# Performance work log

Measured on AMD Instinct MI355X. Metric: run time of the kernel, lower is better.

The kernel has to match this reference:

```python
import jax, jax.numpy as jnp
import numpy as np

CHUNK = 64
MIN_CLAMP = 1e-6
EPS = 1e-5


def layer_norm(x, scale, bias):
    mu = jnp.mean(x, axis=-1, keepdims=True)
    var = jnp.var(x, axis=-1, keepdims=True)
    return (x - mu) / jnp.sqrt(var + EPS) * scale + bias


def group_norm(x, scale, bias, num_groups):
    # Faithful to the module's GroupNorm: stats over (all rows, within-group channels)
    shp = x.shape
    xr = x.reshape(-1, num_groups, shp[-1] // num_groups)
    mu = jnp.mean(xr, axis=(0, 2), keepdims=True)
    var = jnp.var(xr, axis=(0, 2), keepdims=True)
    xn = ((xr - mu) / jnp.sqrt(var + EPS)).reshape(shp)
    return xn * scale + bias


def time_shift(x):
    return jnp.pad(x[:, :-1], ((0, 0), (1, 0), (0, 0)))


def chunkwise_single(k, v, r, w, u, state):
    # one (batch*head) lane: k,v,r,w,u are (L, D); state is (D, D)
    C = CHUNK
    L, D = r.shape
    pad = (-L) % C
    if pad:
        padf = lambda a: jnp.pad(a, ((0, pad), (0, 0)))
        r, k, v, w, u = map(padf, (r, k, v, w, u))
    Lp = L + pad
    N = Lp // C
    r, k, v, w, u = (a.reshape(N, C, D) for a in (r, k, v, w, u))
    w = jnp.log(jnp.clip(w, MIN_CLAMP, 1.0))
    A = jnp.exp(jnp.cumsum(w, axis=1))                                    # (N,C,D)
    A_inter = jnp.exp(jax.lax.cumsum(w, axis=1, reverse=True) - w)        # (N,C,D)
    A_intra = jnp.cumsum(w, axis=1)                                       # (N,C,D)
    kv = jnp.einsum('ncj,nck->ncjk', A_inter * k, v)                      # (N,C,D,D)

    def scan_fn(s, inp):
        A_t, kv_t = inp
        return A_t * s + kv_t, s

    new_state, S = jax.lax.scan(scan_fn, state, (A.reshape(Lp, D), kv.reshape(Lp, D, D)))
    S = S.reshape(N, C, D, D)
    inter = jnp.einsum('ncj,ncjk->nck', r * jnp.exp(A_intra - w), S)

    mid = C // 2

    def intra_fn(rc, kc, vc, Ac, uc):
        r_decay = rc * jnp.exp(jnp.pad(Ac[:-1], ((1, 0), (0, 0))) - Ac[mid:mid + 1])
        k_decay = kc * jnp.exp(Ac[mid:mid + 1] - Ac)
        u_diag = jnp.diag(jnp.sum(rc * uc * kc, -1))
        return (jnp.tril(r_decay @ k_decay.T, -1) + u_diag) @ vc

    intra = jax.vmap(intra_fn)(r, k, v, A_intra, u)
    y = (inter + intra).reshape(Lp, D)[:L]
    return y, new_state


def _forward(x, state, time_maa_x, time_maa_w, time_maa_k, time_maa_v, time_maa_r, time_maa_g,
             time_decay, time_faaaa, time_maa_w1, time_maa_w2, time_decay_w1, time_decay_w2,
             Wr, Wk, Wv, Wg, Wo, ln_x_scale, ln_x_bias,
             time_maa_k_ch, time_maa_r_ch, Wk_ch, Wv_ch, Wr_ch,
             ln1_scale, ln1_bias, ln2_scale, ln2_bias):
    B, T, E = x.shape
    H, Sh = time_faaaa.shape
    # ---- time mixing (on ln1(x)) ----
    xn = layer_norm(x, ln1_scale, ln1_bias)
    sx = time_shift(xn) - xn
    xmix = xn + sx * time_maa_x
    t5 = jnp.tanh(xmix @ time_maa_w1).reshape(B, T, 5, -1).swapaxes(1, 2)    # (B,5,T,32)
    # faithful to original: batched matmul then reshape (B,5,T,E) -> (5,B,T,E)
    m = jnp.einsum('bgtc,gce->bgte', t5, time_maa_w2).reshape(5, B, T, E)
    mw, mk, mv, mr, mg = m
    xw = xn + sx * (time_maa_w + mw)
    xk = xn + sx * (time_maa_k + mk)
    xv = xn + sx * (time_maa_v + mv)
    xr = xn + sx * (time_maa_r + mr)
    xg = xn + sx * (time_maa_g + mg)
    r = (xr @ Wr).reshape(B, T, H, Sh)
    k = (xk @ Wk).reshape(B, T, H, Sh)
    v = (xv @ Wv).reshape(B, T, H, Sh)
    g = jax.nn.silu(xg @ Wg)                                                 # (B,T,H*Sh)
    off = (jnp.tanh(xw @ time_decay_w1) @ time_decay_w2).reshape(B, T, H, Sh)
    w = jax.nn.softplus(-(time_decay.reshape(1, 1, H, Sh) + off))
    u = jnp.broadcast_to(time_faaaa, (B, T, H, Sh))
    lane = lambda a: a.transpose(0, 2, 1, 3).reshape(B * H, T, Sh)
    y, new_state = jax.vmap(chunkwise_single)(lane(k), lane(v), lane(r), lane(w), lane(u),
                                              state.reshape(B * H, Sh, Sh))
    y = y.reshape(B, H, T, Sh).transpose(0, 2, 1, 3).reshape(B, T, H * Sh)
    y = group_norm(y, ln_x_scale, ln_x_bias, H)
    x = x + (y * g) @ Wo
    # ---- channel mixing (on ln2(x)) ----
    xn2 = layer_norm(x, ln2_scale, ln2_bias)
    sx2 = time_shift(xn2) - xn2
    kk = jax.nn.relu((xn2 + sx2 * time_maa_k_ch) @ Wk_ch) ** 2
    kv = kk @ Wv_ch
    out = x + jax.nn.sigmoid((xn2 + sx2 * time_maa_r_ch) @ Wr_ch) * kv
    return out, new_state.reshape(B, H, Sh, Sh)


def setup_inputs():
    B, T, E = 2, 512, 1024
    H, Sh, F = 16, 64, 4096
    D = H * Sh
    layer_id, n_layer = 12, 24
    r01 = layer_id / (n_layer - 1)
    r10 = 1.0 - layer_id / n_layer
    ar_e = np.arange(E, dtype=np.float64) / E
    maa = lambda p: jnp.asarray((1.0 - ar_e ** p).reshape(1, 1, E), jnp.float32)
    n = np.arange(D, dtype=np.float64)
    time_decay = jnp.asarray((-6 + 5 * (n / (D - 1)) ** (0.7 + 1.3 * r01)).reshape(1, D), jnp.float32)
    time_faaaa = jnp.asarray((r01 * (1 - n / (D - 1)) + ((n + 1) % 3 - 1) * 0.1).reshape(H, Sh), jnp.float32)
    key = jax.random.key(0)
    ks = jax.random.split(key, 14)
    uni = lambda kk, shp: jax.random.uniform(kk, shp, jnp.float32, 0.0, 1e-4)
    dense = lambda kk, i, o: jax.random.normal(kk, (i, o), jnp.float32) / np.float32(np.sqrt(i))
    return dict(
        x=jax.random.normal(ks[0], (B, T, E), jnp.float32),
        state=jnp.zeros((B, H, Sh, Sh), jnp.float32),
        time_maa_x=maa(r10), time_maa_w=maa(r10), time_maa_k=maa(r10),
        time_maa_v=maa(r10 + 0.3 * r01), time_maa_r=maa(0.5 * r10), time_maa_g=maa(0.5 * r10),
        time_decay=time_decay, time_faaaa=time_faaaa,
        time_maa_w1=uni(ks[1], (E, 5 * 32)), time_maa_w2=uni(ks[2], (5, 32, E)),
        time_decay_w1=uni(ks[3], (E, 64)), time_decay_w2=uni(ks[4], (64, E)),
        Wr=dense(ks[5], E, D), Wk=dense(ks[6], E, D), Wv=dense(ks[7], E, D),
        Wg=dense(ks[8], E, D), Wo=dense(ks[9], D, E),
        ln_x_scale=jnp.ones((D,), jnp.float32), ln_x_bias=jnp.zeros((D,), jnp.float32),
        time_maa_k_ch=maa(r10), time_maa_r_ch=maa(r10),
        Wk_ch=dense(ks[10], E, F), Wv_ch=dense(ks[11], F, E), Wr_ch=dense(ks[12], E, E),
        ln1_scale=jnp.ones((E,), jnp.float32), ln1_bias=jnp.zeros((E,), jnp.float32),
        ln2_scale=jnp.ones((E,), jnp.float32), ln2_bias=jnp.zeros((E,), jnp.float32),
    )


def reference(x, state, time_maa_x, time_maa_w, time_maa_k, time_maa_v, time_maa_r, time_maa_g,
              time_decay, time_faaaa, time_maa_w1, time_maa_w2, time_decay_w1, time_decay_w2,
              Wr, Wk, Wv, Wg, Wo, ln_x_scale, ln_x_bias,
              time_maa_k_ch, time_maa_r_ch, Wk_ch, Wv_ch, Wr_ch,
              ln1_scale, ln1_bias, ln2_scale, ln2_bias):
    return _forward(x, state, time_maa_x, time_maa_w, time_maa_k, time_maa_v, time_maa_r, time_maa_g,
                    time_decay, time_faaaa, time_maa_w1, time_maa_w2, time_decay_w1, time_decay_w2,
                    Wr, Wk, Wv, Wg, Wo, ln_x_scale, ln_x_bias,
                    time_maa_k_ch, time_maa_r_ch, Wk_ch, Wv_ch, Wr_ch,
                    ln1_scale, ln1_bias, ln2_scale, ln2_bias)
```

## Files before the change

kernel.cpp:

```cpp
#include <hip/hip_runtime.h>
#include <math.h>

#define T_  512
#define E_  1024
#define BTE 1048576

enum { EPI_NONE=0, EPI_TANH=1, EPI_SILU=2, EPI_RELU2=3, EPI_WLOG=4, EPI_ADDRES=5,
       EPI_SIGMUL4=6 };

typedef __attribute__((ext_vector_type(8))) short bf16x8;
typedef __attribute__((ext_vector_type(4))) float f32x4;

__device__ __forceinline__ unsigned short f2bf(float f) {
    union { float f; unsigned u; } v; v.f = f;
    unsigned r = v.u + 0x7fffu + ((v.u >> 16) & 1u);
    return (unsigned short)(r >> 16);
}
__device__ __forceinline__ float bf2f(unsigned short h) {
    union { unsigned u; float f; } v; v.u = ((unsigned)h) << 16;
    return v.f;
}

__global__ __launch_bounds__(256) void ln1mix_k(const float* __restrict__ x,
        const float* __restrict__ sc, const float* __restrict__ bi,
        const float* __restrict__ maa,
        float* __restrict__ xn, unsigned short* __restrict__ xmix)
{
    const int row = blockIdx.x;
    const int t = row & 511;
    const int tid = threadIdx.x;
    const float* xr = x + (size_t)row * E_;
    float4 v = *reinterpret_cast<const float4*>(xr + tid*4);
    float4 vp = make_float4(0.f, 0.f, 0.f, 0.f);
    if (t) vp = *reinterpret_cast<const float4*>(xr - E_ + tid*4);
    float s   = v.x + v.y + v.z + v.w;
    float ss  = v.x*v.x + v.y*v.y + v.z*v.z + v.w*v.w;
    float sp  = vp.x + vp.y + vp.z + vp.w;
    float ssp = vp.x*vp.x + vp.y*vp.y + vp.z*vp.z + vp.w*vp.w;
    #pragma unroll
    for (int off = 32; off > 0; off >>= 1) {
        s   += __shfl_down(s, off);
        ss  += __shfl_down(ss, off);
        sp  += __shfl_down(sp, off);
        ssp += __shfl_down(ssp, off);
    }
    __shared__ float p0[4], p1[4], p2[4], p3[4];
    __shared__ float st[4];
    if ((tid & 63) == 0) { p0[tid>>6]=s; p1[tid>>6]=ss; p2[tid>>6]=sp; p3[tid>>6]=ssp; }
    __syncthreads();
    if (tid == 0) {
        float S  = p0[0]+p0[1]+p0[2]+p0[3];
        float SS = p1[0]+p1[1]+p1[2]+p1[3];
        float Sp = p2[0]+p2[1]+p2[2]+p2[3];
        float SSp= p3[0]+p3[1]+p3[2]+p3[3];
        float mu  = S * (1.f/E_);
        float var = SS * (1.f/E_) - mu*mu;
        float mup = Sp * (1.f/E_);
        float varp= SSp * (1.f/E_) - mup*mup;
        st[0] = mu; st[1] = rsqrtf(var + 1e-5f);
        st[2] = mup; st[3] = rsqrtf(varp + 1e-5f);
    }
    __syncthreads();
    const float mu = st[0], rstd = st[1], mup = st[2], rstdp = st[3];
    float4 s4 = *reinterpret_cast<const float4*>(sc + tid*4);
    float4 b4 = *reinterpret_cast<const float4*>(bi + tid*4);
    float xnv[4], prv[4];
    xnv[0]=(v.x-mu)*rstd*s4.x+b4.x; xnv[1]=(v.y-mu)*rstd*s4.y+b4.y;
    xnv[2]=(v.z-mu)*rstd*s4.z+b4.z; xnv[3]=(v.w-mu)*rstd*s4.w+b4.w;
    prv[0]=t?(vp.x-mup)*rstdp*s4.x+b4.x:0.f; prv[1]=t?(vp.y-mup)*rstdp*s4.y+b4.y:0.f;
    prv[2]=t?(vp.z-mup)*rstdp*s4.z+b4.z:0.f; prv[3]=t?(vp.w-mup)*rstdp*s4.w+b4.w:0.f;
    float4 o; o.x=xnv[0]; o.y=xnv[1]; o.z=xnv[2]; o.w=xnv[3];
    *reinterpret_cast<float4*>(xn + (size_t)row*E_ + tid*4) = o;
    #pragma unroll
    for (int j = 0; j < 4; ++j) {
        int e = tid*4 + j;
        xmix[(size_t)row*E_ + e] = f2bf(xnv[j] + (prv[j]-xnv[j])*maa[e]);
    }
}

__global__ __launch_bounds__(256) void ln2mix_k(const float* __restrict__ x2,
        const float* __restrict__ sc, const float* __restrict__ bi,
        const float* __restrict__ maaK, const float* __restrict__ maaR,
        unsigned short* __restrict__ ak, unsigned short* __restrict__ ar)
{
    const int row = blockIdx.x;
    const int t = row & 511;
    const int tid = threadIdx.x;
    const float* xr = x2 + (size_t)row * E_;
    float4 v = *reinterpret_cast<const float4*>(xr + tid*4);
    float4 vp = make_float4(0.f, 0.f, 0.f, 0.f);
    if (t) vp = *reinterpret_cast<const float4*>(xr - E_ + tid*4);
    float s   = v.x + v.y + v.z + v.w;
    float ss  = v.x*v.x + v.y*v.y + v.z*v.z + v.w*v.w;
    float sp  = vp.x + vp.y + vp.z + vp.w;
    float ssp = vp.x*vp.x + vp.y*vp.y + vp.z*vp.z + vp.w*vp.w;
    #pragma unroll
    for (int off = 32; off > 0; off >>= 1) {
        s   += __shfl_down(s, off);
        ss  += __shfl_down(ss, off);
        sp  += __shfl_down(sp, off);
        ssp += __shfl_down(ssp, off);
    }
    __shared__ float p0[4], p1[4], p2[4], p3[4];
    __shared__ float st[4];
    if ((tid & 63) == 0) { p0[tid>>6]=s; p1[tid>>6]=ss; p2[tid>>6]=sp; p3[tid>>6]=ssp; }
    __syncthreads();
    if (tid == 0) {
        float S  = p0[0]+p0[1]+p0[2]+p0[3];
        float SS = p1[0]+p1[1]+p1[2]+p1[3];
        float Sp = p2[0]+p2[1]+p2[2]+p2[3];
        float SSp= p3[0]+p3[1]+p3[2]+p3[3];
        float mu  = S * (1.f/E_);
        float var = SS * (1.f/E_) - mu*mu;
        float mup = Sp * (1.f/E_);
        float varp= SSp * (1.f/E_) - mup*mup;
        st[0] = mu; st[1] = rsqrtf(var + 1e-5f);
        st[2] = mup; st[3] = rsqrtf(varp + 1e-5f);
    }
    __syncthreads();
    const float mu = st[0], rstd = st[1], mup = st[2], rstdp = st[3];
    float4 s4 = *reinterpret_cast<const float4*>(sc + tid*4);
    float4 b4 = *reinterpret_cast<const float4*>(bi + tid*4);
    float xnv[4], prv[4];
    xnv[0]=(v.x-mu)*rstd*s4.x+b4.x; xnv[1]=(v.y-mu)*rstd*s4.y+b4.y;
    xnv[2]=(v.z-mu)*rstd*s4.z+b4.z; xnv[3]=(v.w-mu)*rstd*s4.w+b4.w;
    prv[0]=t?(vp.x-mup)*rstdp*s4.x+b4.x:0.f; prv[1]=t?(vp.y-mup)*rstdp*s4.y+b4.y:0.f;
    prv[2]=t?(vp.z-mup)*rstdp*s4.z+b4.z:0.f; prv[3]=t?(vp.w-mup)*rstdp*s4.w+b4.w:0.f;
    #pragma unroll
    for (int j = 0; j < 4; ++j) {
        int e = tid*4 + j;
        float sxv = prv[j] - xnv[j];
        ak[(size_t)row*E_ + e] = f2bf(xnv[j] + sxv*maaK[e]);
        ar[(size_t)row*E_ + e] = f2bf(xnv[j] + sxv*maaR[e]);
    }
}

__global__ __launch_bounds__(256) void t5red_k(const float* __restrict__ tp,
        unsigned short* __restrict__ t5p)
{
    int idx = blockIdx.x*256 + threadIdx.x;
    int c = idx & 63, bt = (idx >> 6) & 1023, g = idx >> 16;
    unsigned short o = 0;
    if (c < 32) {
        float s = 0.f;
        size_t off = (size_t)bt*160 + g*32 + c;
        #pragma unroll
        for (int z = 0; z < 8; ++z) s += tp[(size_t)z*163840 + off];
        o = f2bf(tanhf(s));
    }
    t5p[idx] = o;
}

__global__ __launch_bounds__(256) void dw1red_k(const float* __restrict__ dp,
        unsigned short* __restrict__ h)
{
    int idx = blockIdx.x*256 + threadIdx.x;
    float s = 0.f;
    #pragma unroll
    for (int z = 0; z < 8; ++z) s += dp[(size_t)z*65536 + idx];
    h[idx] = f2bf(tanhf(s));
}

__global__ __launch_bounds__(256) void mix5_apply_k(const float* __restrict__ xn,
        const unsigned short* __restrict__ mb,
        const float* __restrict__ maaW, const float* __restrict__ maaK,
        const float* __restrict__ maaV, const float* __restrict__ maaR,
        const float* __restrict__ maaG,
        unsigned short* __restrict__ xw, unsigned short* __restrict__ xk,
        unsigned short* __restrict__ xv, unsigned short* __restrict__ xr,
        unsigned short* __restrict__ xg)
{
    int idx = blockIdx.x*256 + threadIdx.x;
    int e = idx & 1023;
    int bt = idx >> 10;
    int b = bt >> 9, t = bt & 511;
    float xnv = xn[idx];
    float prev = t ? xn[idx - E_] : 0.f;
    float sxv = prev - xnv;
    float m[5];
    #pragma unroll
    for (int o = 0; o < 5; ++o) {
        int L = o*2 + b;
        int bs = L / 5, gs = L - bs*5;
        m[o] = bf2f(mb[(size_t)gs*1048576 + (size_t)(bs*T_ + t)*E_ + e]);
    }
    xw[idx] = f2bf(xnv + sxv*(maaW[e] + m[0]));
    xk[idx] = f2bf(xnv + sxv*(maaK[e] + m[1]));
    xv[idx] = f2bf(xnv + sxv*(maaV[e] + m[2]));
    xr[idx] = f2bf(xnv + sxv*(maaR[e] + m[3]));
    xg[idx] = f2bf(xnv + sxv*(maaG[e] + m[4]));
}

struct WTA {
    const float* src[16];
    unsigned short* dst[16];
    int K[16], N[16], Npad[16], Kpad[16], tx[16];
    int cum[17];
};
__global__ __launch_bounds__(256) void wtransall_k(WTA a)
{
    int bid = blockIdx.x;
    int s = 0;
    while (bid >= a.cum[s+1]) ++s;
    const int local = bid - a.cum[s];
    const int bx = local % a.tx[s];
    const int by = local / a.tx[s];
    const float* S = a.src[s];
    unsigned short* D = a.dst[s];
    const int K = a.K[s], N = a.N[s], Npad = a.Npad[s], Kpad = a.Kpad[s];
    __shared__ float t[64][65];
    const int tid = threadIdx.x;
    const int k0 = by*64, n0 = bx*64;
    #pragma unroll
    for (int i = 0; i < 16; ++i) {
        int r = i*4 + (tid >> 6), c = tid & 63;
        int gk = k0 + r, gn = n0 + c;
        t[r][c] = (gk < K && gn < N) ? S[(size_t)gk*N + gn] : 0.f;
    }
    __syncthreads();
    #pragma unroll
    for (int i = 0; i < 16; ++i) {
        int r = i*4 + (tid >> 6), c = tid & 63;
        int gn = n0 + r, gk = k0 + c;
        if (gn < Npad && gk < Kpad)
            D[(size_t)gn*Kpad + gk] = f2bf(t[c][r]);
    }
}

struct GemmArgs {
    const unsigned short* A[8];
    const unsigned short* B[8];
    void* C[8];
    const float* p1[8];
    const float* p2[8];
    int epi[8];
    int obf[8];
    int k0[8];
    int M, N, K, ldK;
};
__global__ __launch_bounds__(256) void mgemm_k(GemmArgs g)
{
    const int bz = blockIdx.z;
    const unsigned short* Ag = g.A[bz];
    const unsigned short* BT = g.B[bz];
    const int N = g.N, K = g.K;
    const int gx = gridDim.x, gy = gridDim.y;
    const int lin = blockIdx.x + gx*blockIdx.y;
    const int q = (gx*gy) >> 3;
    const int tile = (lin & 7)*q + (lin >> 3);
    const int bx = tile / gy;
    const int by = tile - bx*gy;
    const int m0 = by * 64, n0 = bx * 64;
    const int tid = threadIdx.x;
    const int lane = tid & 63, w = tid >> 6;

    __shared__ __align__(16) unsigned short As[2][4096];
    __shared__ __align__(16) unsigned short Bs[2][4096];

    const size_t rowBytes = (size_t)g.ldK * 2;
    int sI[4], sIsB[4]; size_t sOff[4];
    #pragma unroll
    for (int ii = 0; ii < 4; ++ii) {
        int t = w*4 + ii;
        int isB = t >> 3;
        int i = t & 7;
        int r = i*8 + (lane >> 3);
        int gb = ((lane & 7) * 16) ^ ((r & 7) << 4);
        sI[ii] = i; sIsB[ii] = isB;
        int srow = (isB ? n0 : m0) + r;
        sOff[ii] = (size_t)srow * rowBytes + gb;
    }
    auto stage = [&](int buf, size_t kbyte) {
        #pragma unroll
        for (int ii = 0; ii < 4; ++ii) {
            const char* src = (const char*)(sIsB[ii] ? BT : Ag) + sOff[ii] + kbyte;
            unsigned short* dst = (sIsB[ii] ? Bs[buf] : As[buf]) + sI[ii]*512;
            auto g1 = (const __attribute__((address_space(1))) unsigned int*)(src);
            auto l3 = (__attribute__((address_space(3))) unsigned int*)(uintptr_t)(dst);
            __builtin_amdgcn_global_load_lds(g1, l3, 16, 0, 0);
        }
    };

    const int wm = (w >> 1) * 32, wn = (w & 1) * 32;
    const int lr = lane & 15, lk = lane >> 4;
    int aoff[2][2], boff[2][2];
    #pragma unroll
    for (int mi = 0; mi < 2; ++mi)
        #pragma unroll
        for (int kw = 0; kw < 2; ++kw) {
            int ar = wm + mi*16 + lr;
            aoff[mi][kw] = ar*128 + ((kw*64 + lk*16) ^ ((ar & 7) << 4));
            int br = wn + mi*16 + lr;
            boff[mi][kw] = br*128 + ((kw*64 + lk*16) ^ ((br & 7) << 4));
        }

    f32x4 acc[2][2] = {};
    const size_t kbase = (size_t)g.k0[bz] * 2;
    stage(0, kbase);
    const int nk = K >> 6;
    int cur = 0;
    for (int kt = 0; kt < nk; ++kt) {
        __syncthreads();
        if (kt + 1 < nk) stage(cur ^ 1, kbase + (size_t)(kt + 1) * 128);
        const char* Ab = (const char*)As[cur];
        const char* Bb = (const char*)Bs[cur];
        bf16x8 af[2][2], bfv[2][2];
        #pragma unroll
        for (int mi = 0; mi < 2; ++mi)
            #pragma unroll
            for (int kw = 0; kw < 2; ++kw) {
                af[mi][kw]  = *(const bf16x8*)(Ab + aoff[mi][kw]);
                bfv[mi][kw] = *(const bf16x8*)(Bb + boff[mi][kw]);
            }
        #pragma unroll
        for (int kw = 0; kw < 2; ++kw)
            #pragma unroll
            for (int mi = 0; mi < 2; ++mi)
                #pragma unroll
                for (int ni = 0; ni < 2; ++ni)
                    acc[mi][ni] = __builtin_amdgcn_mfma_f32_16x16x32_bf16(
                        af[mi][kw], bfv[ni][kw], acc[mi][ni], 0, 0, 0);
        cur ^= 1;
    }

    const int epi = g.epi[bz], obf = g.obf[bz];
    const float* p1 = g.p1[bz];
    const float* p2 = g.p2[bz];
    float* Cf = (float*)g.C[bz];
    unsigned short* Ch = (unsigned short*)g.C[bz];
    #pragma unroll
    for (int mi = 0; mi < 2; ++mi) {
        #pragma unroll
        for (int ni = 0; ni < 2; ++ni) {
            #pragma unroll
            for (int j = 0; j < 4; ++j) {
                int gm = m0 + wm + mi*16 + lk*4 + j;
                int gn = n0 + wn + ni*16 + lr;
                if (gn >= N) continue;
                size_t idx = (size_t)gm * N + gn;
                float a = acc[mi][ni][j];
                float o = a;
                if (epi == EPI_TANH)        o = tanhf(a);
                else if (epi == EPI_SILU)   o = a / (1.f + expf(-a));
                else if (epi == EPI_RELU2)  { float r = fmaxf(a, 0.f); o = r*r; }
                else if (epi == EPI_WLOG) {
                    float z = -(p1[gn] + a);
                    float sp = (z > 15.f) ? z : log1pf(expf(z));
                    o = logf(fminf(fmaxf(sp, 1e-6f), 1.f));
                }
                else if (epi == EPI_ADDRES) o = a + p1[idx];
                else if (epi == EPI_SIGMUL4) {
                    float kvs = p1[idx] + p1[idx + BTE] + p1[idx + 2*BTE] + p1[idx + 3*BTE];
                    o = p2[idx] + kvs / (1.f + expf(-a));
                }
                if (obf) Ch[idx] = f2bf(o); else Cf[idx] = o;
            }
        }
    }
}

#define SWZI(r, c)  (((r) << 6) + ((c) ^ (((r) & 7) << 3)))
#define FIDX(r, kw) (((r) << 6) + ((((kw)*32) + fk*8) ^ (((r) & 7) << 3)))
__global__ __launch_bounds__(1024, 4) void chunk1_k(
    const unsigned short* __restrict__ rb, const unsigned short* __restrict__ kb,
    const unsigned short* __restrict__ vb,
    const unsigned short* __restrict__ hdecb, const unsigned short* __restrict__ dw2T,
    const float* __restrict__ tdecay, const float* __restrict__ faaaa,
    float* __restrict__ ypart, unsigned short* __restrict__ Ug,
    unsigned short* __restrict__ RDimg, unsigned short* __restrict__ BFb,
    float* __restrict__ B63g)
{
    const int blk = blockIdx.x;
    const int bh = blk >> 3, nc = blk & 7;
    const int b = bh >> 4, h = bh & 15;
    const int tid = threadIdx.x;
    const int l = tid & 63, w = tid >> 6;
    const int jl = l, q = w;
    const int fr = l & 15, fk = l >> 4;
    const int wm = (w >> 2) * 16, wn = (w & 3) * 16;
    const int t0 = nc * 64;

    __shared__ float sQS[16][64];
    __shared__ float sUD[64];
    __shared__ __align__(16) unsigned short pool[32768];
    unsigned short* sRDb  = pool;
    unsigned short* sKAb  = pool + 4096;
    unsigned short* sKA2b = pool + 8192;
    unsigned short* sKATb = pool + 12288;
    unsigned short* sVTb  = pool + 16384;
    unsigned short* sVXTb = pool + 20480;
    unsigned short* sQMb  = pool + 24576;
    unsigned short* sPMb  = pool + 28672;
    float* wlogf = (float*)(pool + 12288);

    const float u_reg = faaaa[h*64 + jl];
    const size_t base = (size_t)b*T_*E_ + (size_t)h*64;
    const size_t coff = (size_t)blk * 4096;

    {
        const int isB = w >> 3;
        const int i = w & 7;
        const int r = i*8 + (l >> 3);
        const int gb = ((l & 7)*16) ^ ((r & 7) << 4);
        const char* src = isB
            ? ((const char*)dw2T  + (size_t)(h*64 + r)*128 + gb)
            : ((const char*)hdecb + (size_t)(b*T_ + t0 + r)*128 + gb);
        unsigned short* dst = (isB ? sPMb : sQMb) + i*512;
        auto g1 = (const __attribute__((address_space(1))) unsigned int*)(src);
        auto l3 = (__attribute__((address_space(3))) unsigned int*)(uintptr_t)(dst);
        __builtin_amdgcn_global_load_lds(g1, l3, 16, 0, 0);
    }
    __syncthreads();

    {
        f32x4 accO = {};
        #pragma unroll
        for (int kw = 0; kw < 2; ++kw) {
            bf16x8 aH = *(const bf16x8*)(&sQMb[FIDX(wm + fr, kw)]);
            bf16x8 bD = *(const bf16x8*)(&sPMb[FIDX(wn + fr, kw)]);
            accO = __builtin_amdgcn_mfma_f32_16x16x32_bf16(aH, bD, accO, 0,0,0);
        }
        const float td = tdecay[h*64 + wn + fr];
        #pragma unroll
        for (int reg = 0; reg < 4; ++reg) {
            const int t = wm + fk*4 + reg;
            const int col = wn + fr;
            float z = -(td + accO[reg]);
            float sp = (z > 15.f) ? z : log1pf(expf(z));
            wlogf[t*64 + col] = logf(fminf(fmaxf(sp, 1e-6f), 1.f));
        }
    }
    __syncthreads();

    float loc[4], vreg[4];
    {
        float cum = 0.f;
        #pragma unroll
        for (int c = 0; c < 4; ++c) {
            float wv = wlogf[(q*4 + c)*64 + jl];
            cum += wv; loc[c] = cum;
        }
        sQS[q][jl] = cum;
    }
    __syncthreads();
    float pre = 0.f, atot = 0.f;
    #pragma unroll
    for (int qq = 0; qq < 16; ++qq) {
        float v = sQS[qq][jl];
        atot += v;
        if (qq < q) pre += v;
    }

    #pragma unroll
    for (int c = 0; c < 4; ++c) {
        const int t = q*4 + c;
        const size_t gi = base + (size_t)(t0 + t)*E_ + jl;
        const float rv = bf2f(rb[gi]), kv = bf2f(kb[gi]), vv = bf2f(vb[gi]);
        vreg[c] = vv;
        const float a = loc[c] + pre;
        const float aprev = (c > 0) ? (loc[c-1] + pre) : pre;
        sRDb [SWZI(t, jl)] = f2bf(rv * expf(aprev));
        const float ka = kv * expf(atot - a);
        sKAb [SWZI(t, jl)] = f2bf(ka);
        sKA2b[SWZI(t, jl)] = f2bf(kv * expf(-a));
        sKATb[SWZI(jl, t)] = f2bf(ka);
        sVTb [SWZI(jl, t)] = f2bf(vv);
        float p = rv * u_reg * kv;
        #pragma unroll
        for (int off = 32; off > 0; off >>= 1) p += __shfl_down(p, off);
        if (jl == 0) sUD[t] = p;
    }
    __syncthreads();

    f32x4 accQ = {}, accP = {};
    #pragma unroll
    for (int kw = 0; kw < 2; ++kw) {
        bf16x8 ar  = *(const bf16x8*)(&sRDb [FIDX(wm + fr, kw)]);
        bf16x8 bka = *(const bf16x8*)(&sKAb [FIDX(wn + fr, kw)]);
        bf16x8 bk2 = *(const bf16x8*)(&sKA2b[FIDX(wn + fr, kw)]);
        accQ = __builtin_amdgcn_mfma_f32_16x16x32_bf16(ar, bk2, accQ, 0,0,0);
        accP = __builtin_amdgcn_mfma_f32_16x16x32_bf16(ar, bka, accP, 0,0,0);
    }
    #pragma unroll
    for (int reg = 0; reg < 4; ++reg) {
        int t = wm + fk*4 + reg;
        int s = wn + fr;
        float qv = (s < t) ? accQ[reg] : ((s == t) ? sUD[t] : 0.f);
        float pv = (s < t) ? accP[reg] : 0.f;
        sQMb[SWZI(t, s)] = f2bf(qv);
        sPMb[SWZI(t, s)] = f2bf(pv);
    }

    float loc2[4];
    {
        float cum2 = 0.f;
        #pragma unroll
        for (int c = 0; c < 4; ++c) {
            cum2 += loc[c] + pre;
            loc2[c] = cum2;
        }
        sQS[q][jl] = cum2;
    }
    __syncthreads();
    {
        float pre2 = 0.f;
        #pragma unroll
        for (int qq = 0; qq < 16; ++qq) if (qq < q) pre2 += sQS[qq][jl];
        #pragma unroll
        for (int c = 0; c < 4; ++c) {
            const int t = q*4 + c;
            const float Bv = loc2[c] + pre2;
            const float Bprev = (c > 0) ? (loc2[c-1] + pre2) : pre2;
            const unsigned short bfh = f2bf(expf(Bprev));
            sKA2b[t*64 + jl] = bfh;
            BFb[coff + t*64 + jl] = bfh;
            sVXTb[SWZI(jl, t)] = f2bf(vreg[c] * expf(-Bv));
            if (t == 63) B63g[(size_t)blk*64 + jl] = expf(Bv);
        }
    }
    __syncthreads();

    {
        f32x4 accI = {}, accL = {}, accU = {};
        #pragma unroll
        for (int kw = 0; kw < 2; ++kw) {
            bf16x8 aQ = *(const bf16x8*)(&sQMb [FIDX(wm + fr, kw)]);
            bf16x8 aP = *(const bf16x8*)(&sPMb [FIDX(wm + fr, kw)]);
            bf16x8 aK = *(const bf16x8*)(&sKATb[FIDX(wm + fr, kw)]);
            bf16x8 bV = *(const bf16x8*)(&sVTb [FIDX(wn + fr, kw)]);
            bf16x8 bX = *(const bf16x8*)(&sVXTb[FIDX(wn + fr, kw)]);
            accI = __builtin_amdgcn_mfma_f32_16x16x32_bf16(aQ, bV, accI, 0,0,0);
            accL = __builtin_amdgcn_mfma_f32_16x16x32_bf16(aP, bX, accL, 0,0,0);
            accU = __builtin_amdgcn_mfma_f32_16x16x32_bf16(aK, bX, accU, 0,0,0);
        }
        #pragma unroll
        for (int reg = 0; reg < 4; ++reg) {
            int t = wm + fk*4 + reg;
            int k = wn + fr;
            float bfv = bf2f(sKA2b[t*64 + k]);
            ypart[base + (size_t)(t0 + t)*E_ + k] = accI[reg] + bfv*accL[reg];
            Ug[coff + t*64 + k] = f2bf(accU[reg]);
        }
    }
    if (tid < 512)
        ((bf16x8*)(RDimg + coff))[tid] = ((const bf16x8*)sRDb)[tid];
}

__global__ __launch_bounds__(256) void chunk2_k(
    const float* __restrict__ st_in, const unsigned short* __restrict__ Ug,
    const float* __restrict__ B63g,
    unsigned short* __restrict__ Simg, float* __restrict__ st_out)
{
    const int bh = blockIdx.x;
    const int tid = threadIdx.x;
    __shared__ float S[4096];
    for (int i = tid; i < 4096; i += 256) S[i] = st_in[(size_t)bh*4096 + i];
    __syncthreads();
    const int k = tid >> 2, j0 = (tid & 3) * 16;
    for (int nc = 0; nc < 8; ++nc) {
        const size_t coff = ((size_t)bh*8 + nc) * 4096;
        #pragma unroll
        for (int hf = 0; hf < 2; ++hf) {
            bf16x8 tmp;
            #pragma unroll
            for (int e = 0; e < 8; ++e) tmp[e] = (short)f2bf(S[(j0 + hf*8 + e)*64 + k]);
            *(bf16x8*)(&Simg[coff + SWZI(k, j0 + hf*8)]) = tmp;
        }
        __syncthreads();
        for (int i = tid; i < 4096; i += 256) {
            int kk = i & 63;
            S[i] = B63g[((size_t)bh*8 + nc)*64 + kk] * (S[i] + bf2f(Ug[coff + i]));
        }
        __syncthreads();
    }
    for (int i = tid; i < 4096; i += 256) st_out[(size_t)bh*4096 + i] = S[i];
}

__global__ __launch_bounds__(256) void chunk3_k(
    const unsigned short* __restrict__ RDimg, const unsigned short* __restrict__ Simg,
    const unsigned short* __restrict__ BFb, float* __restrict__ yb,
    float* __restrict__ part)
{
    const int blk = blockIdx.x;
    const int bh = blk >> 3, nc = blk & 7;
    const int b = bh >> 4, h = bh & 15;
    const int tid = threadIdx.x;
    const int l = tid & 63, w = tid >> 6;
    const int fr = l & 15, fk = l >> 4;
    const int wm = (w >> 1) * 32, wn = (w & 1) * 32;
    const int t0 = nc * 64;
    __shared__ __align__(16) unsigned short sRDb[4096];
    __shared__ __align__(16) unsigned short sSTb[4096];
    const size_t coff = (size_t)blk * 4096;

    #pragma unroll
    for (int ii = 0; ii < 2; ++ii) {
        int seg = (w*2 + ii) * 512;
        {
            auto g1 = (const __attribute__((address_space(1))) unsigned int*)(RDimg + coff + seg + (l << 3));
            auto l3 = (__attribute__((address_space(3))) unsigned int*)(uintptr_t)(sRDb + seg);
            __builtin_amdgcn_global_load_lds(g1, l3, 16, 0, 0);
        }
        {
            auto g1 = (const __attribute__((address_space(1))) unsigned int*)(Simg + coff + seg + (l << 3));
            auto l3 = (__attribute__((address_space(3))) unsigned int*)(uintptr_t)(sSTb + seg);
            __builtin_amdgcn_global_load_lds(g1, l3, 0x10, 0, 0);
        }
    }
    __syncthreads();

    f32x4 accS[2][2] = {};
    #pragma unroll
    for (int kw = 0; kw < 2; ++kw) {
        bf16x8 aR[2], bS[2];
        #pragma unroll
        for (int mi = 0; mi < 2; ++mi)
            aR[mi] = *(const bf16x8*)(&sRDb[FIDX(wm + mi*16 + fr, kw)]);
        #pragma unroll
        for (int ni = 0; ni < 2; ++ni)
            bS[ni] = *(const bf16x8*)(&sSTb[FIDX(wn + ni*16 + fr, kw)]);
        #pragma unroll
        for (int mi = 0; mi < 2; ++mi)
            #pragma unroll
            for (int ni = 0; ni < 2; ++ni)
                accS[mi][ni] = __builtin_amdgcn_mfma_f32_16x16x32_bf16(aR[mi], bS[ni], accS[mi][ni], 0,0,0);
    }
    const size_t base = (size_t)b*T_*E_ + (size_t)h*64;
    float s = 0.f, ss = 0.f;
    #pragma unroll
    for (int mi = 0; mi < 2; ++mi)
        #pragma unroll
        for (int ni = 0; ni < 2; ++ni)
            #pragma unroll
            for (int reg = 0; reg < 4; ++reg) {
                int t = wm + mi*16 + fk*4 + reg;
                int k = wn + ni*16 + fr;
                size_t gp = base + (size_t)(t0 + t)*E_ + k;
                float yv = yb[gp] + bf2f(BFb[coff + t*64 + k]) * accS[mi][ni][reg];
                yb[gp] = yv;
                s += yv; ss += yv*yv;
            }
    #pragma unroll
    for (int off = 32; off > 0; off >>= 1) {
        s  += __shfl_down(s, off);
        ss += __shfl_down(ss, off);
    }
    __shared__ float ps[4], pss[4];
    if (l == 0) { ps[w] = s; pss[w] = ss; }
    __syncthreads();
    if (tid == 0) {
        part[blk]       = ps[0]+ps[1]+ps[2]+ps[3];
        part[256 + blk] = pss[0]+pss[1]+pss[2]+pss[3];
    }
}

__global__ __launch_bounds__(256) void gn_apply_k(const float* __restrict__ y,
        const float* __restrict__ g, const float* __restrict__ part,
        const float* __restrict__ sc, const float* __restrict__ bi,
        unsigned short* __restrict__ z)
{
    __shared__ float smu[16], srs[16];
    const int tid = threadIdx.x;
    if (tid < 16) {
        float s = 0.f, ss = 0.f;
        #pragma unroll
        for (int b = 0; b < 2; ++b)
            #pragma unroll
            for (int ncc = 0; ncc < 8; ++ncc) {
                int ib = (b*16 + tid)*8 + ncc;
                s  += part[ib];
                ss += part[256 + ib];
            }
        float mu  = s * (1.f/65536.f);
        float var = ss * (1.f/65536.f) - mu*mu;
        smu[tid] = mu;
        srs[tid] = rsqrtf(var + 1e-5f);
    }
    __syncthreads();
    int idx = blockIdx.x*256 + tid;
    int d = idx & 1023;
    int h = d >> 6;
    float yn = (y[idx] - smu[h])*srs[h]*sc[d] + bi[d];
    z[idx] = f2bf(yn * g[idx]);
}

extern "C" void kernel_launch(void* const* d_in, const int* in_sizes, int n_in,
                              void* d_out, int out_size, void* d_ws, size_t ws_size,
                              hipStream_t stream)
{
    const float* x       = (const float*)d_in[0];
    const float* state0  = (const float*)d_in[1];
    const float* maa_x   = (const float*)d_in[2];
    const float* maa_w   = (const float*)d_in[3];
    const float* maa_k   = (const float*)d_in[4];
    const float* maa_v   = (const float*)d_in[5];
    const float* maa_r   = (const float*)d_in[6];
    const float* maa_g   = (const float*)d_in[7];
    const float* tdecay  = (const float*)d_in[8];
    const float* faaaa   = (const float*)d_in[9];
    const float* w1      = (const float*)d_in[10];
    const float* w2      = (const float*)d_in[11];
    const float* dw1     = (const float*)d_in[12];
    const float* dw2     = (const float*)d_in[13];
    const float* Wr      = (const float*)d_in[14];
    const float* Wk      = (const float*)d_in[15];
    const float* Wv      = (const float*)d_in[16];
    const float* Wg      = (const float*)d_in[17];
    const float* Wo      = (const float*)d_in[18];
    const float* lnx_s   = (const float*)d_in[19];
    const float* lnx_b   = (const float*)d_in[20];
    const float* maa_kch = (const float*)d_in[21];
    const float* maa_rch = (const float*)d_in[22];
    const float* Wk_ch   = (const float*)d_in[23];
    const float* Wv_ch   = (const float*)d_in[24];
    const float* Wr_ch   = (const float*)d_in[25];
    const float* ln1_s   = (const float*)d_in[26];
    const float* ln1_b   = (const float*)d_in[27];
    const float* ln2_s   = (const float*)d_in[28];
    const float* ln2_b   = (const float*)d_in[29];

    float* xn     = (float*)d_ws;
    float* t5dead = xn + 1048576;
    float* gbuf   = t5dead + 163840;
    float* wlogb  = gbuf + 1048576;
    float* ybuf   = wlogb + 1048576;
    float* kvb    = ybuf + 1048576;
    float* gnpart = kvb + 1048576;
    float* gnstat = gnpart + 1024;
    float* b63g   = gnstat + 32;
    unsigned short* u = (unsigned short*)(b63g + 16384);
    unsigned short* xmix = u;  u += 1048576;
    unsigned short* xw   = u;  u += 1048576;
    unsigned short* xk   = u;  u += 1048576;
    unsigned short* xv_  = u;  u += 1048576;
    unsigned short* xr   = u;  u += 1048576;
    unsigned short* xg   = u;  u += 1048576;
    unsigned short* xtr  = u;  u += 1048576;
    unsigned short* rb   = u;  u += 1048576;
    unsigned short* kb   = u;  u += 1048576;
    unsigned short* vb   = u;  u += 1048576;
    unsigned short* hdecb= u;  u += 65536;
    unsigned short* WrT  = u;  u += 1048576;
    unsigned short* WkT  = u;  u += 1048576;
    unsigned short* WvT  = u;  u += 1048576;
    unsigned short* WgT  = u;  u += 1048576;
    unsigned short* WoT  = u;  u += 1048576;
    unsigned short* WrchT= u;  u += 1048576;
    unsigned short* WkchT= u;  u += 4194304;
    unsigned short* WvchT= u;  u += 4194304;
    unsigned short* w1T  = u;  u += 196608;
    unsigned short* dw1T = u;  u += 65536;
    unsigned short* dw2T = u;  u += 65536;
    unsigned short* W2T5 = u;  u += 327680;
    unsigned short* t5p  = u;  u += 327680;
    unsigned short* zbuf  = xmix;
    unsigned short* akb   = xw;
    unsigned short* arb   = xk;
    unsigned short* kkb   = xv_;
    unsigned short* mb16  = (unsigned short*)wlogb;
    unsigned short* Ug    = xv_;
    unsigned short* RDimg = xg;
    unsigned short* Simg  = xtr;
    unsigned short* BFb   = xmix;
    float* tpart = gbuf;
    float* dpart = (float*)xmix;
    float* kpart = gbuf;

    float* out   = (float*)d_out;
    float* x2buf = out;
    float* stout = out + (size_t)BTE;

    {
        WTA a{};
        const float* srcs[16] = {Wr, Wk, Wv, Wg, Wo, Wr_ch, Wk_ch, Wv_ch, w1, dw1, dw2,
                                 w2, w2+32768, w2+65536, w2+98304, w2+131072};
        unsigned short* dsts[16] = {WrT, WkT, WvT, WgT, WoT, WrchT, WkchT, WvchT,
                                    w1T, dw1T, dw2T,
                                    W2T5, W2T5+65536, W2T5+131072, W2T5+196608, W2T5+262144};
        int Ks[16]    = {1024,1024,1024,1024,1024,1024, 1024, 4096, 1024, 1024,   64, 32,32,32,32,32};
        int Ns[16]    = {1024,1024,1024,1024,1024,1024, 4096, 1024,  160,   64, 1024, 1024,1024,1024,1024,1024};
        int Npads[16] = {1024,1024,1024,1024,1024,1024, 4096, 1024,  192,   64, 1024, 1024,1024,1024,1024,1024};
        int Kpads[16] = {1024,1024,1024,1024,1024,1024, 1024, 4096, 1024, 1024,   64, 64,64,64,64,64};
        int cum = 0;
        for (int i = 0; i < 16; ++i) {
            a.src[i] = srcs[i]; a.dst[i] = dsts[i];
            a.K[i] = Ks[i]; a.N[i] = Ns[i]; a.Npad[i] = Npads[i]; a.Kpad[i] = Kpads[i];
            int txc = (Ns[i] + 63) / 64;
            int tyc = (Ks[i] + 63) / 64;
            a.tx[i] = txc;
            a.cum[i] = cum;
            cum += txc * tyc;
        }
        a.cum[16] = cum;
        wtransall_k<<<cum, 256, 0, stream>>>(a);
    }

    ln1mix_k<<<1024, 256, 0, stream>>>(x, ln1_s, ln1_b, maa_x, xn, xmix);
    { GemmArgs g{}; g.M=1024; g.N=160; g.K=128; g.ldK=1024;
      for (int z = 0; z < 8; ++z) {
          g.A[z]=xmix; g.B[z]=w1T; g.C[z]=tpart + (size_t)z*163840;
          g.epi[z]=EPI_NONE; g.obf[z]=0; g.k0[z]=z*128;
      }
      mgemm_k<<<dim3(3,16,8), 256, 0, stream>>>(g); }
    t5red_k<<<1280, 256, 0, stream>>>(tpart, t5p);
    { GemmArgs g{}; g.M=1024; g.N=1024; g.K=64; g.ldK=64;
      for (int z = 0; z < 5; ++z) {
          g.A[z]=t5p + (size_t)z*65536; g.B[z]=W2T5 + (size_t)z*65536;
          g.C[z]=mb16 + (size_t)z*1048576; g.epi[z]=EPI_NONE; g.obf[z]=1;
      }
      mgemm_k<<<dim3(16,16,5), 256, 0, stream>>>(g); }
    mix5_apply_k<<<4096, 256, 0, stream>>>(xn, mb16, maa_w, maa_k, maa_v, maa_r, maa_g,
                                           xw, xk, xv_, xr, xg);
    { GemmArgs g{}; g.M=1024; g.N=1024; g.K=1024; g.ldK=1024;
      g.A[0]=xr;  g.B[0]=WrT; g.C[0]=rb;   g.epi[0]=EPI_NONE; g.obf[0]=1;
      g.A[1]=xk;  g.B[1]=WkT; g.C[1]=kb;   g.epi[1]=EPI_NONE; g.obf[1]=1;
      g.A[2]=xv_; g.B[2]=WvT; g.C[2]=vb;   g.epi[2]=EPI_NONE; g.obf[2]=1;
      g.A[3]=xg;  g.B[3]=WgT; g.C[3]=gbuf; g.epi[3]=EPI_SILU; g.obf[3]=0;
      mgemm_k<<<dim3(16,16,4), 256, 0, stream>>>(g); }
    { GemmArgs g{}; g.M=1024; g.N=64; g.K=128; g.ldK=1024;
      for (int z = 0; z < 8; ++z) {
          g.A[z]=xw; g.B[z]=dw1T; g.C[z]=dpart + (size_t)z*65536;
          g.epi[z]=EPI_NONE; g.obf[z]=0; g.k0[z]=z*128;
      }
      mgemm_k<<<dim3(1,16,8), 256, 0, stream>>>(g); }
    dw1red_k<<<256, 256, 0, stream>>>(dpart, hdecb);

    chunk1_k<<<256, 1024, 0, stream>>>(rb, kb, vb, hdecb, dw2T, tdecay, faaaa,
                                       ybuf, Ug, RDimg, BFb, b63g);
    chunk2_k<<<32, 256, 0, stream>>>(state0, Ug, b63g, Simg, stout);
    chunk3_k<<<256, 256, 0, stream>>>(RDimg, Simg, BFb, ybuf, gnpart);

    gn_apply_k<<<4096, 256, 0, stream>>>(ybuf, gbuf, gnpart, lnx_s, lnx_b, zbuf);
    { GemmArgs g{}; g.M=1024; g.N=1024; g.K=1024; g.ldK=1024;
      g.A[0]=zbuf; g.B[0]=WoT; g.C[0]=x2buf; g.epi[0]=EPI_ADDRES; g.obf[0]=0; g.p1[0]=x;
      mgemm_k<<<dim3(16,16,1), 256, 0, stream>>>(g); }

    ln2mix_k<<<1024, 256, 0, stream>>>(x2buf, ln2_s, ln2_b, maa_kch, maa_rch, akb, arb);
    { GemmArgs g{}; g.M=1024; g.N=4096; g.K=1024; g.ldK=1024;
      g.A[0]=akb; g.B[0]=WkchT; g.C[0]=kkb; g.epi[0]=EPI_RELU2; g.obf[0]=1;
      mgemm_k<<<dim3(64,16,1), 256, 0, stream>>>(g); }
    { GemmArgs g{}; g.M=1024; g.N=1024; g.K=1024; g.ldK=4096;
      for (int z = 0; z < 4; ++z) {
          g.A[z]=kkb; g.B[z]=WvchT; g.C[z]=kpart + (size_t)z*BTE;
          g.epi[z]=EPI_NONE; g.obf[z]=0; g.k0[z]=z*1024;
      }
      mgemm_k<<<dim3(16,16,4), 256, 0, stream>>>(g); }
    { GemmArgs g{}; g.M=1024; g.N=1024; g.K=1024; g.ldK=1024;
      g.A[0]=arb; g.B[0]=WrchT; g.C[0]=out; g.epi[0]=EPI_SIGMUL4; g.obf[0]=0;
      g.p1[0]=kpart; g.p2[0]=x2buf;
      mgemm_k<<<dim3(16,16,1), 256, 0, stream>>>(g); }
}
```

Baseline: 186.1 us.

## Split-K the output projection GEMM and fold reduction plus residual into ln2mix

Result: no change. 184.9 us (median of 2 runs) (-0.7%).

```diff
diff --git a/kernel.cpp b/kernel.cpp
--- a/kernel.cpp
+++ b/kernel.cpp
@@ -78,38 +78,52 @@
     }
 }
 
-__global__ __launch_bounds__(256) void ln2mix_k(const float* __restrict__ x2,
+__global__ __launch_bounds__(256) void ln2mix_k(const float* __restrict__ pa,
+        const float* __restrict__ pb, const float* __restrict__ xres,
         const float* __restrict__ sc, const float* __restrict__ bi,
         const float* __restrict__ maaK, const float* __restrict__ maaR,
+        float* __restrict__ x2out,
         unsigned short* __restrict__ ak, unsigned short* __restrict__ ar)
 {
     const int row = blockIdx.x;
     const int t = row & 511;
     const int tid = threadIdx.x;
-    const float* xr = x2 + (size_t)row * E_;
-    float4 v = *reinterpret_cast<const float4*>(xr + tid*4);
+    const size_t off = (size_t)row*E_ + tid*4;
+    float4 a0 = *reinterpret_cast<const float4*>(pa + off);
+    float4 a1 = *reinterpret_cast<const float4*>(pb + off);
+    float4 xv = *reinterpret_cast<const float4*>(xres + off);
+    float4 v;
+    v.x = a0.x + a1.x + xv.x; v.y = a0.y + a1.y + xv.y;
+    v.z = a0.z + a1.z + xv.z; v.w = a0.w + a1.w + xv.w;
     float4 vp = make_float4(0.f, 0.f, 0.f, 0.f);
-    if (t) vp = *reinterpret_cast<const float4*>(xr - E_ + tid*4);
+    if (t) {
+        float4 b0 = *reinterpret_cast<const float4*>(pa + off - E_);
+        float4 b1 = *reinterpret_cast<const float4*>(pb + off - E_);
+        float4 bx = *reinterpret_cast<const float4*>(xres + off - E_);
+        vp.x = b0.x + b1.x + bx.x; vp.y = b0.y + b1.y + bx.y;
+        vp.z = b0.z + b1.z + bx.z; vp.w = b0.w + b1.w + bx.w;
+    }
+    *reinterpret_cast<float4*>(x2out + off) = v;
     float s   = v.x + v.y + v.z + v.w;
     float ss  = v.x*v.x + v.y*v.y + v.z*v.z + v.w*v.w;
     float sp  = vp.x + vp.y + vp.z + vp.w;
     float ssp = vp.x*vp.x + vp.y*vp.y + vp.z*vp.z + vp.w*vp.w;
     #pragma unroll
-    for (int off = 32; off > 0; off >>= 1) {
-        s   += __shfl_down(s, off);
-        ss  += __shfl_down(ss, off);
-        sp  += __shfl_down(sp, off);
-        ssp += __shfl_down(ssp, off);
-    }
-    __shared__ float p0[4], p1[4], p2[4], p3[4];
+    for (int off2 = 32; off2 > 0; off2 >>= 1) {
+        s   += __shfl_down(s, off2);
+        ss  += __shfl_down(ss, off2);
+        sp  += __shfl_down(sp, off2);
+        ssp += __shfl_down(ssp, off2);
+    }
+    __shared__ float q0[4], q1[4], q2[4], q3[4];
     __shared__ float st[4];
-    if ((tid & 63) == 0) { p0[tid>>6]=s; p1[tid>>6]=ss; p2[tid>>6]=sp; p3[tid>>6]=ssp; }
+    if ((tid & 63) == 0) { q0[tid>>6]=s; q1[tid>>6]=ss; q2[tid>>6]=sp; q3[tid>>6]=ssp; }
     __syncthreads();
     if (tid == 0) {
-        float S  = p0[0]+p0[1]+p0[2]+p0[3];
-        float SS = p1[0]+p1[1]+p1[2]+p1[3];
-        float Sp = p2[0]+p2[1]+p2[2]+p2[3];
-        float SSp= p3[0]+p3[1]+p3[2]+p3[3];
+        float S  = q0[0]+q0[1]+q0[2]+q0[3];
+        float SS = q1[0]+q1[1]+q1[2]+q1[3];
+        float Sp = q2[0]+q2[1]+q2[2]+q2[3];
+        float SSp= q3[0]+q3[1]+q3[2]+q3[3];
         float mu  = S * (1.f/E_);
         float var = SS * (1.f/E_) - mu*mu;
         float mup = Sp * (1.f/E_);
@@ -397,6 +411,13 @@
     const size_t base = (size_t)b*T_*E_ + (size_t)h*64;
     const size_t coff = (size_t)blk * 4096;
 
+    unsigned short rh[4], kh[4], vh[4];
+    #pragma unroll
+    for (int c = 0; c < 4; ++c) {
+        const size_t gi = base + (size_t)(t0 + q*4 + c)*E_ + jl;
+        rh[c] = rb[gi]; kh[c] = kb[gi]; vh[c] = vb[gi];
+    }
+
     {
         const int isB = w >> 3;
         const int i = w & 7;
@@ -454,8 +475,7 @@
     #pragma unroll
     for (int c = 0; c < 4; ++c) {
         const int t = q*4 + c;
-        const size_t gi = base + (size_t)(t0 + t)*E_ + jl;
-        const float rv = bf2f(rb[gi]), kv = bf2f(kb[gi]), vv = bf2f(vb[gi]);
+        const float rv = bf2f(rh[c]), kv = bf2f(kh[c]), vv = bf2f(vh[c]);
         vreg[c] = vv;
         const float a = loc[c] + pre;
         const float aprev = (c > 0) ? (loc[c-1] + pre) : pre;
@@ -604,7 +624,7 @@
         {
             auto g1 = (const __attribute__((address_space(1))) unsigned int*)(Simg + coff + seg + (l << 3));
             auto l3 = (__attribute__((address_space(3))) unsigned int*)(uintptr_t)(sSTb + seg);
-            __builtin_amdgcn_global_load_lds(g1, l3, 0x10, 0, 0);
+            __builtin_amdgcn_global_load_lds(g1, l3, 16, 0, 0);
         }
     }
     __syncthreads();
@@ -765,6 +785,8 @@
     float* tpart = gbuf;
     float* dpart = (float*)xmix;
     float* kpart = gbuf;
+    float* wop0  = wlogb;
+    float* wop1  = ybuf;
 
     float* out   = (float*)d_out;
     float* x2buf = out;
@@ -831,11 +853,13 @@
     chunk3_k<<<256, 256, 0, stream>>>(RDimg, Simg, BFb, ybuf, gnpart);
 
     gn_apply_k<<<4096, 256, 0, stream>>>(ybuf, gbuf, gnpart, lnx_s, lnx_b, zbuf);
-    { GemmArgs g{}; g.M=1024; g.N=1024; g.K=1024; g.ldK=1024;
-      g.A[0]=zbuf; g.B[0]=WoT; g.C[0]=x2buf; g.epi[0]=EPI_ADDRES; g.obf[0]=0; g.p1[0]=x;
-      mgemm_k<<<dim3(16,16,1), 256, 0, stream>>>(g); }
-
-    ln2mix_k<<<1024, 256, 0, stream>>>(x2buf, ln2_s, ln2_b, maa_kch, maa_rch, akb, arb);
+    { GemmArgs g{}; g.M=1024; g.N=1024; g.K=512; g.ldK=1024;
+      g.A[0]=zbuf; g.B[0]=WoT; g.C[0]=wop0; g.epi[0]=EPI_NONE; g.obf[0]=0; g.k0[0]=0;
+      g.A[1]=zbuf; g.B[1]=WoT; g.C[1]=wop1; g.epi[1]=EPI_NONE; g.obf[1]=0; g.k0[1]=512;
+      mgemm_k<<<dim3(16,16,2), 256, 0, stream>>>(g); }
+
+    ln2mix_k<<<1024, 256, 0, stream>>>(wop0, wop1, x, ln2_s, ln2_b,
+                                       maa_kch, maa_rch, x2buf, akb, arb);
     { GemmArgs g{}; g.M=1024; g.N=4096; g.K=1024; g.ldK=1024;
       g.A[0]=akb; g.B[0]=WkchT; g.C[0]=kkb; g.epi[0]=EPI_RELU2; g.obf[0]=1;
       mgemm_k<<<dim3(64,16,1), 256, 0, stream>>>(g); }
```
